# Kernel tuning notes

Hardware: AMD Instinct MI355X
Metric: run time of the kernel (lower is better)

Reference implementation:

```python
import jax, jax.numpy as jnp
import numpy as np

DIM = 512
NUM_HEADS = 16
WIN = (7, 7)
N = WIN[0] * WIN[1]          # 49 tokens per window
NW = 64                      # windows per image
B = 32                       # images
B_ = B * NW                  # total windows = 2048
SCALE = (DIM // NUM_HEADS) ** -0.5


def _relative_position_index(wh, ww):
    coords = np.stack(np.meshgrid(np.arange(wh), np.arange(ww), indexing='ij'))  # (2, wh, ww)
    coords = coords.reshape(2, -1)                                               # (2, N)
    rel = coords[:, :, None] - coords[:, None, :]                                # (2, N, N)
    rel = rel.transpose(1, 2, 0).astype(np.int32)                                # (N, N, 2)
    rel[:, :, 0] += wh - 1
    rel[:, :, 1] += ww - 1
    rel[:, :, 0] *= 2 * ww - 1
    return jnp.asarray(rel.sum(-1), dtype=jnp.int32)                             # (N, N)


def _shift_mask(nw, n):
    # Swin-style additive mask: 0 within groups, -100 across groups.
    rng = np.random.RandomState(0)
    groups = rng.randint(0, 4, size=(nw, n)).astype(np.int32)
    m = np.where(groups[:, :, None] == groups[:, None, :], 0.0, -100.0)
    return jnp.asarray(m, dtype=jnp.float32)                                     # (nW, N, N)


def setup_inputs() -> dict:
    key = jax.random.key(0)
    ks = jax.random.split(key, 5)
    x = jax.random.normal(ks[0], (B_, N, DIM), dtype=jnp.float32)
    qkv_w = jax.random.normal(ks[1], (3 * DIM, DIM), dtype=jnp.float32) * 0.02
    qkv_b = jnp.zeros((3 * DIM,), dtype=jnp.float32)
    proj_w = jax.random.normal(ks[2], (DIM, DIM), dtype=jnp.float32) * 0.02
    proj_b = jnp.zeros((DIM,), dtype=jnp.float32)
    rpb_table = jax.random.normal(ks[3], ((2 * WIN[0] - 1) * (2 * WIN[1] - 1), NUM_HEADS), dtype=jnp.float32) * 0.02
    mask = _shift_mask(NW, N)
    rel_idx = _relative_position_index(*WIN)
    return {"x": x, "mask": mask, "qkv_w": qkv_w, "qkv_b": qkv_b,
            "proj_w": proj_w, "proj_b": proj_b, "rpb_table": rpb_table,
            "rel_idx": rel_idx}


def reference(x, mask, qkv_w, qkv_b, proj_w, proj_b, rpb_table, rel_idx):
    b_, n, c = x.shape
    nh = rpb_table.shape[1]
    d = c // nh
    # qkv projection: (B_, N, 3, nH, d) -> q, k, v each (B_, nH, N, d)
    qkv = (jnp.einsum('bnc,oc->bno', x, qkv_w) + qkv_b).reshape(b_, n, 3, nh, d)
    qkv = jnp.transpose(qkv, (2, 0, 3, 1, 4))
    q, k, v = qkv[0], qkv[1], qkv[2]
    attn = jnp.einsum('bhnd,bhmd->bhnm', q * SCALE, k)                     # (B_, nH, N, N)
    # gathered relative position bias: (N*N, nH) -> (nH, N, N)
    bias = rpb_table[rel_idx.reshape(-1)].reshape(n, n, nh)
    attn = attn + jnp.transpose(bias, (2, 0, 1))[None]
    # shifted-window mask add
    nw = mask.shape[0]
    attn = attn.reshape(b_ // nw, nw, nh, n, n) + mask[None, :, None]
    attn = attn.reshape(b_, nh, n, n)
    attn = jax.nn.softmax(attn, axis=-1)
    out = jnp.einsum('bhnm,bhmd->bhnd', attn, v)                           # (B_, nH, N, d)
    out = jnp.transpose(out, (0, 2, 1, 3)).reshape(b_, n, c)
    return jnp.einsum('bnc,oc->bno', out, proj_w) + proj_b
```

## Files before the change

### kernel.cpp

```cpp
#include <hip/hip_runtime.h>
#include <hip/hip_bf16.h>
#include <stdint.h>
#include <stddef.h>

#define B_TOT   2048
#define NTOK    49
#define CDIM    512
#define NHEAD   16
#define HD      32
#define NWIN    64
#define MROWS   (B_TOT*NTOK)
#define O_QKV   1536
#define SCALE_F 0.17677669529663687f

typedef short bf16x8 __attribute__((ext_vector_type(8)));
typedef float f32x4  __attribute__((ext_vector_type(4)));

__device__ __forceinline__ unsigned short f2bf(float f){
  union { float f; unsigned u; } v; v.f = f;
  unsigned r = v.u + 0x7fffu + ((v.u >> 16) & 1u);
  return (unsigned short)(r >> 16);
}
__device__ __forceinline__ unsigned pkbf(float a, float b){
  return (unsigned)f2bf(a) | ((unsigned)f2bf(b) << 16);
}

#define GL16(g,l) __builtin_amdgcn_global_load_lds( \
      (const __attribute__((address_space(1))) unsigned int*)(g), \
      (__attribute__((address_space(3))) unsigned int*)(l), 16, 0, 0)

__global__ void k_prep(const float* __restrict__ x,
                       const float* __restrict__ qkv_w, const float* __restrict__ proj_w,
                       const float* __restrict__ rpb, const int* __restrict__ rel_idx,
                       const float* __restrict__ mask,
                       unsigned short* __restrict__ xb,
                       unsigned short* __restrict__ wqkv, unsigned short* __restrict__ wproj,
                       float* __restrict__ bmb){
  int i = blockIdx.x * blockDim.x + threadIdx.x;
  int st = gridDim.x * blockDim.x;
  const int n4 = MROWS * CDIM / 4;
  for (int j = i; j < n4; j += st){
    float4 v = ((const float4*)x)[j];
    uint2 o;
    o.x = pkbf(v.x, v.y);
    o.y = pkbf(v.z, v.w);
    ((uint2*)xb)[j] = o;
  }
  for (int j = i; j < O_QKV*CDIM; j += st) wqkv[j] = f2bf(qkv_w[j]);
  for (int j = i; j < CDIM*CDIM;  j += st) wproj[j] = f2bf(proj_w[j]);
  const int TOT = NWIN * NHEAD * NTOK * 64;
  for (int j = i; j < TOT; j += st){
    int wh  = j / (NTOK*64);
    int rem = j - wh * (NTOK*64);
    int qt  = rem >> 6, kt = rem & 63;
    int wi = wh >> 4, h = wh & 15;
    float v;
    if (kt < NTOK){
      int rc = qt * NTOK + kt;
      v = mask[wi * (NTOK*NTOK) + rc] + rpb[rel_idx[rc] * NHEAD + h];
    } else v = -1e30f;
    bmb[j] = v;
  }
}

#define LDA_(P,RG,MI,S) (*(const bf16x8*)(rA + (P)*32768 + (RG)*16384 + (MI)*2048 + ((S)?(cb0^64):cb0)))
#define LDB_(P,CG,NI,S) (*(const bf16x8*)(rB + (P)*32768 + (CG)*16384 + (NI)*2048 + ((S)?(cb0^64):cb0)))

#define RDA(P,RG)  { _Pragma("unroll") for (int mi=0;mi<4;++mi){ af[mi][0]=LDA_(P,RG,mi,0); af[mi][1]=LDA_(P,RG,mi,1);} }
#define RDB0(P,CG) { _Pragma("unroll") for (int ni=0;ni<2;++ni){ bfr0[ni][0]=LDB_(P,CG,ni,0); bfr0[ni][1]=LDB_(P,CG,ni,1);} }
#define RDB1(P,CG) { _Pragma("unroll") for (int ni=0;ni<2;++ni){ bfr1[ni][0]=LDB_(P,CG,ni,0); bfr1[ni][1]=LDB_(P,CG,ni,1);} }

#define STAGE_A(P,HG,KT) { \
    GL16(aS0 + (size_t)(HG)*64*Kb + (size_t)(KT)*128, ldA + (P)*32768 + (HG)*16384); \
    GL16(aS1 + (size_t)(HG)*64*Kb + (size_t)(KT)*128, ldA + (P)*32768 + (HG)*16384 + 8192); }
#define STAGE_B(P,HG,KT) { \
    GL16(bS0 + (size_t)(HG)*32*Kb + (size_t)(KT)*128, ldB + (P)*32768 + (HG)*16384); \
    GL16(bS1 + (size_t)(HG)*32*Kb + (size_t)(KT)*128, ldB + (P)*32768 + (HG)*16384 + 8192); }

#define PH2(PRE,RG,VM) { \
  PRE; \
  __builtin_amdgcn_s_barrier(); \
  asm volatile("s_waitcnt lgkmcnt(0)" ::: "memory"); \
  __builtin_amdgcn_sched_barrier(0); \
  __builtin_amdgcn_s_setprio(1); \
  _Pragma("unroll") for (int s=0;s<2;++s) \
    _Pragma("unroll") for (int mi=0;mi<4;++mi){ \
      _Pragma("unroll") for (int ni=0;ni<2;++ni) \
        acc[(RG)*4+mi][ni] = __builtin_amdgcn_mfma_f32_16x16x32_bf16(af[mi][s], bfr0[ni][s], acc[(RG)*4+mi][ni], 0,0,0); \
      _Pragma("unroll") for (int ni=0;ni<2;++ni) \
        acc[(RG)*4+mi][2+ni] = __builtin_amdgcn_mfma_f32_16x16x32_bf16(af[mi][s], bfr1[ni][s], acc[(RG)*4+mi][2+ni], 0,0,0); \
    } \
  __builtin_amdgcn_s_setprio(0); \
  if (VM) asm volatile("s_waitcnt vmcnt(4)" ::: "memory"); \
  __builtin_amdgcn_s_barrier(); \
  asm volatile("" ::: "memory"); \
}

template<int OUT_F32>
__global__ __launch_bounds__(512, 2) void k_gemm8(const unsigned short* __restrict__ Ag,
                                                  const unsigned short* __restrict__ Bg,
                                                  const float* __restrict__ bias,
                                                  void* __restrict__ Cout,
                                                  int Ndim, int Kdim){
  extern __shared__ char smem[];
  const int tid = threadIdx.x;
  const int wv = tid >> 6, lane = tid & 63, lg = lane >> 4, lr = lane & 15;
  const int wm = wv >> 2, wn = wv & 3;

  const int nbx = gridDim.x;
  const int nwg = nbx * gridDim.y;
  const int id  = blockIdx.y * nbx + blockIdx.x;
  const int nid = (id & 7) * (nwg >> 3) + (id >> 3);
  const int bx = nid % nbx, by = nid / nbx;
  const int bm0 = by * 256, bn0 = bx * 256;
  const size_t Kb = (size_t)Kdim * 2;
  const int NIT = Kdim >> 7;

  const int srow = tid >> 3;
  const int scb  = ((tid & 7) << 4) ^ ((srow & 7) << 4);
  const char* aS0 = (const char*)Ag + (size_t)(bm0 + srow) * Kb + scb;
  const char* aS1 = (const char*)Ag + (size_t)(bm0 + 128 + srow) * Kb + scb;
  const char* bS0 = (const char*)Bg + (size_t)(bn0 + (srow>>5)*64 + (srow&31)) * Kb + scb;
  const char* bS1 = (const char*)Bg + (size_t)(bn0 + 128 + (srow>>5)*64 + (srow&31)) * Kb + scb;
  char* ldA = smem + wv * 1024;
  char* ldB = smem + 65536 + wv * 1024;

  const int cb0 = (lg * 16) ^ ((lr & 7) << 4);
  const char* rA = smem + (wm*64 + lr) * 128;
  const char* rB = smem + 65536 + (wn*32 + lr) * 128;

  f32x4 acc[8][4];
  #pragma unroll
  for (int i = 0; i < 8; ++i)
    #pragma unroll
    for (int j = 0; j < 4; ++j)
      #pragma unroll
      for (int r = 0; r < 4; ++r) acc[i][j][r] = 0.f;

  bf16x8 af[4][2], bfr0[2][2], bfr1[2][2];

  STAGE_A(0,0,0); STAGE_A(0,1,0); STAGE_B(0,0,0); STAGE_B(0,1,0);
  STAGE_A(1,0,1); STAGE_B(1,1,1);
  asm volatile("s_waitcnt vmcnt(4)" ::: "memory");
  __builtin_amdgcn_s_barrier();
  asm volatile("" ::: "memory");

  for (int it = 0; it < NIT; ++it){
    const int T = 2*it;
    PH2( RDA(0,0); RDB0(0,0); RDB1(0,1); STAGE_A(1,1,(T+1)); STAGE_B(1,0,(T+1)), 0, 0)
    PH2( RDA(0,1); STAGE_A(0,0,(T+2)); STAGE_B(0,1,(T+2)),                        1, 1)
    PH2( RDA(1,0); RDB0(1,0); RDB1(1,1); STAGE_A(0,1,(T+2)); STAGE_B(0,0,(T+2)), 0, 0)
    PH2( RDA(1,1); STAGE_A(1,0,(T+3)); STAGE_B(1,1,(T+3)),                        1, 1)
  }

  #pragma unroll
  for (int RG = 0; RG < 2; ++RG)
    #pragma unroll
    for (int mi = 0; mi < 4; ++mi)
      #pragma unroll
      for (int CG = 0; CG < 2; ++CG)
        #pragma unroll
        for (int ni = 0; ni < 2; ++ni){
          f32x4 v = acc[RG*4+mi][CG*2+ni];
          const int col = bn0 + wn*64 + CG*32 + ni*16 + lr;
          const float bc = bias[col];
          #pragma unroll
          for (int r = 0; r < 4; ++r){
            const int row = bm0 + wm*128 + RG*64 + mi*16 + lg*4 + r;
            const float t = v[r] + bc;
            if (OUT_F32) ((float*)Cout)[(size_t)row * Ndim + col] = t;
            else ((unsigned short*)Cout)[(size_t)row * Ndim + col] = f2bf(t);
          }
        }
}

__global__ __launch_bounds__(256) void k_attn(const unsigned short* __restrict__ qkv,
                                              const float* __restrict__ bm,
                                              unsigned short* __restrict__ ao){
  __shared__ char lds[4][12288];
  const int wv = threadIdx.x >> 6, lane = threadIdx.x & 63;
  const int lg = lane >> 4, lr = lane & 15;
  const int gw = blockIdx.x * 4 + wv;
  const int w = gw >> 4, h = gw & 15, wi = w & (NWIN - 1);
  char* Vt = lds[wv];
  char* P  = lds[wv] + 4096;

  const unsigned short* base = qkv + (size_t)w * NTOK * O_QKV + h * HD;

  const int vkt = lane >> 2, vch = lane & 3;
  bf16x8 vld[4];
  #pragma unroll
  for (int t = 0; t < 4; ++t){
    int kt = 16*t + vkt; int kts = kt < NTOK ? kt : NTOK-1;
    vld[t] = *(const bf16x8*)(base + 1024 + (size_t)kts * O_QKV + vch * 8);
  }

  bf16x8 qf[4], kf[4];
  #pragma unroll
  for (int i = 0; i < 4; ++i){
    int t = 16*i + lr; int ts = t < NTOK ? t : NTOK-1;
    qf[i] = *(const bf16x8*)(base + (size_t)ts * O_QKV + lg*8);
    kf[i] = *(const bf16x8*)(base + 512 + (size_t)ts * O_QKV + lg*8);
  }

  const float* bmp = bm + (size_t)(wi * NHEAD + h) * (NTOK * 64);
  f32x4 bias[4][4];
  #pragma unroll
  for (int mi = 0; mi < 4; ++mi){
    int qt = 16*mi + lr; int qtc = qt < NTOK ? qt : NTOK-1;
    #pragma unroll
    for (int ni = 0; ni < 4; ++ni)
      bias[mi][ni] = *(const f32x4*)(bmp + qtc*64 + ni*16 + lg*4);
  }

  f32x4 z4 = {0.f, 0.f, 0.f, 0.f};
  f32x4 s2[4][4];
  #pragma unroll
  for (int ni = 0; ni < 4; ++ni)
    #pragma unroll
    for (int mi = 0; mi < 4; ++mi)
      s2[ni][mi] = __builtin_amdgcn_mfma_f32_16x16x32_bf16(kf[ni], qf[mi], z4, 0, 0, 0);

  #pragma unroll
  for (int t = 0; t < 4; ++t){
    int kt = 16*t + vkt;
    #pragma unroll
    for (int j = 0; j < 8; ++j){
      int d = vch*8 + j;
      int swz = ((d & 7) ^ (d >> 3)) & 7;
      int byte = d*128 + ((2*kt) ^ (swz << 4));
      *(unsigned short*)(Vt + byte) = (unsigned short)vld[t][j];
    }
  }

  #pragma unroll
  for (int mi = 0; mi < 4; ++mi){
    float v[4][4];
    float mx = -1e30f;
    #pragma unroll
    for (int ni = 0; ni < 4; ++ni)
      #pragma unroll
      for (int r = 0; r < 4; ++r){
        float t = s2[ni][mi][r] * SCALE_F + bias[mi][ni][r];
        v[ni][r] = t;
        mx = fmaxf(mx, t);
      }
    mx = fmaxf(mx, __shfl_xor(mx, 16));
    mx = fmaxf(mx, __shfl_xor(mx, 32));
    float sum = 0.f;
    #pragma unroll
    for (int ni = 0; ni < 4; ++ni)
      #pragma unroll
      for (int r = 0; r < 4; ++r){
        float p = __expf(v[ni][r] - mx);
        v[ni][r] = p;
        sum += p;
      }
    sum += __shfl_xor(sum, 16);
    sum += __shfl_xor(sum, 32);
    float rn = 1.0f / sum;
    const int qt = 16*mi + lr;
    #pragma unroll
    for (int ni = 0; ni < 4; ++ni){
      uint2 pw;
      pw.x = pkbf(v[ni][0]*rn, v[ni][1]*rn);
      pw.y = pkbf(v[ni][2]*rn, v[ni][3]*rn);
      int byte = qt*128 + ((32*ni + 8*lg) ^ ((lr & 7) << 4));
      *(uint2*)(P + byte) = pw;
    }
  }

  f32x4 o[4][2];
  #pragma unroll
  for (int mi = 0; mi < 4; ++mi)
    #pragma unroll
    for (int ni = 0; ni < 2; ++ni)
      #pragma unroll
      for (int r = 0; r < 4; ++r) o[mi][ni][r] = 0.f;

  #pragma unroll
  for (int s = 0; s < 2; ++s){
    bf16x8 pf[4], vf[2];
    #pragma unroll
    for (int mi = 0; mi < 4; ++mi)
      pf[mi] = *(const bf16x8*)(P + (16*mi + lr)*128 + ((64*s + 16*lg) ^ ((lr & 7) << 4)));
    #pragma unroll
    for (int ni = 0; ni < 2; ++ni){
      int d = 16*ni + lr;
      int swz = ((d & 7) ^ (d >> 3)) & 7;
      vf[ni] = *(const bf16x8*)(Vt + d*128 + ((64*s + 16*lg) ^ (swz << 4)));
    }
    #pragma unroll
    for (int mi = 0; mi < 4; ++mi)
      #pragma unroll
      for (int ni = 0; ni < 2; ++ni)
        o[mi][ni] = __builtin_amdgcn_mfma_f32_16x16x32_bf16(pf[mi], vf[ni], o[mi][ni], 0, 0, 0);
  }

  unsigned short* aop = ao + (size_t)w * NTOK * CDIM + h * HD;
  #pragma unroll
  for (int mi = 0; mi < 4; ++mi)
    #pragma unroll
    for (int ni = 0; ni < 2; ++ni)
      #pragma unroll
      for (int r = 0; r < 4; ++r){
        int row = 16*mi + 4*lg + r, col = 16*ni + lr;
        if (row < NTOK)
          aop[(size_t)row * CDIM + col] = f2bf(o[mi][ni][r]);
      }
}

extern "C" void kernel_launch(void* const* d_in, const int* in_sizes, int n_in,
                              void* d_out, int out_size, void* d_ws, size_t ws_size,
                              hipStream_t stream){
  const float* x      = (const float*)d_in[0];
  const float* mask   = (const float*)d_in[1];
  const float* qkv_w  = (const float*)d_in[2];
  const float* qkv_b  = (const float*)d_in[3];
  const float* proj_w = (const float*)d_in[4];
  const float* proj_b = (const float*)d_in[5];
  const float* rpb    = (const float*)d_in[6];
  const int*   rel_i  = (const int*)d_in[7];

  char* ws = (char*)d_ws;
  unsigned short* xb    = (unsigned short*)(ws);
  unsigned short* qkvb  = (unsigned short*)(ws + 102760448);
  unsigned short* wqkv  = (unsigned short*)(ws + 411041792);
  unsigned short* wproj = (unsigned short*)(ws + 412614656);
  float*          bmb   = (float*)(ws + 413138944);

  (void)hipFuncSetAttribute(reinterpret_cast<const void*>(&k_gemm8<0>),
                            hipFuncAttributeMaxDynamicSharedMemorySize, 131072);
  (void)hipFuncSetAttribute(reinterpret_cast<const void*>(&k_gemm8<1>),
                            hipFuncAttributeMaxDynamicSharedMemorySize, 131072);

  k_prep<<<2048, 256, 0, stream>>>(x, qkv_w, proj_w, rpb, rel_i, mask, xb, wqkv, wproj, bmb);
  k_gemm8<0><<<dim3(O_QKV/256, MROWS/256), 512, 131072, stream>>>(xb, wqkv, qkv_b, qkvb, O_QKV, CDIM);
  k_attn<<<(B_TOT * NHEAD) / 4, 256, 0, stream>>>(qkvb, bmb, xb);
  k_gemm8<1><<<dim3(CDIM/256, MROWS/256), 512, 131072, stream>>>(xb, wproj, proj_b, d_out, CDIM, CDIM);
}
```

Measured before the change: 494.8 us.

## Process two adjacent N-tiles per GEMM workgroup with prefetch across tiles

Each GEMM workgroup now computes two consecutive 256-wide output column tiles for the same row block, halving the grid. The last K iteration of the first tile prefetches the first K slices of the next tile's B operand, so the pipeline prologue is overlapped. The intent is to amortize launch/prologue cost and reuse A-row locality in cache, at the cost of fewer workgroups and longer per-block runtime. Correctness relies on the A tile restaging from K=0 and on N being a multiple of 512.

```diff
diff --git a/kernel.cpp b/kernel.cpp
--- a/kernel.cpp
+++ b/kernel.cpp
@@ -76,6 +76,9 @@
 #define STAGE_B(P,HG,KT) { \
     GL16(bS0 + (size_t)(HG)*32*Kb + (size_t)(KT)*128, ldB + (P)*32768 + (HG)*16384); \
     GL16(bS1 + (size_t)(HG)*32*Kb + (size_t)(KT)*128, ldB + (P)*32768 + (HG)*16384 + 8192); }
+#define STAGE_BN(P,HG,KT) { \
+    GL16(bS0 + offD + (size_t)(HG)*32*Kb + (size_t)(KT)*128, ldB + (P)*32768 + (HG)*16384); \
+    GL16(bS1 + offD + (size_t)(HG)*32*Kb + (size_t)(KT)*128, ldB + (P)*32768 + (HG)*16384 + 8192); }
 
 #define PH2(PRE,RG,VM) { \
   PRE; \
@@ -107,12 +110,13 @@
   const int wv = tid >> 6, lane = tid & 63, lg = lane >> 4, lr = lane & 15;
   const int wm = wv >> 2, wn = wv & 3;
 
-  const int nbx = gridDim.x;
-  const int nwg = nbx * gridDim.y;
-  const int id  = blockIdx.y * nbx + blockIdx.x;
-  const int nid = (id & 7) * (nwg >> 3) + (id >> 3);
-  const int bx = nid % nbx, by = nid / nbx;
-  const int bm0 = by * 256, bn0 = bx * 256;
+  const int npairs = gridDim.x;
+  const int b = blockIdx.x;
+  const int pid = (b & 7) * (npairs >> 3) + (b >> 3);
+  const int nbx = Ndim >> 8;
+  const int id0 = pid * 2;
+  const int bx0 = id0 % nbx, by = id0 / nbx;
+  const int bm0 = by * 256;
   const size_t Kb = (size_t)Kdim * 2;
   const int NIT = Kdim >> 7;
 
@@ -120,8 +124,9 @@
   const int scb  = ((tid & 7) << 4) ^ ((srow & 7) << 4);
   const char* aS0 = (const char*)Ag + (size_t)(bm0 + srow) * Kb + scb;
   const char* aS1 = (const char*)Ag + (size_t)(bm0 + 128 + srow) * Kb + scb;
-  const char* bS0 = (const char*)Bg + (size_t)(bn0 + (srow>>5)*64 + (srow&31)) * Kb + scb;
-  const char* bS1 = (const char*)Bg + (size_t)(bn0 + 128 + (srow>>5)*64 + (srow&31)) * Kb + scb;
+  const char* bS0 = (const char*)Bg + (size_t)((bx0 << 8) + (srow>>5)*64 + (srow&31)) * Kb + scb;
+  const char* bS1 = (const char*)Bg + (size_t)((bx0 << 8) + 128 + (srow>>5)*64 + (srow&31)) * Kb + scb;
+  size_t offD = (size_t)256 * Kb;
   char* ldA = smem + wv * 1024;
   char* ldB = smem + 65536 + wv * 1024;
 
@@ -130,13 +135,6 @@
   const char* rB = smem + 65536 + (wn*32 + lr) * 128;
 
   f32x4 acc[8][4];
-  #pragma unroll
-  for (int i = 0; i < 8; ++i)
-    #pragma unroll
-    for (int j = 0; j < 4; ++j)
-      #pragma unroll
-      for (int r = 0; r < 4; ++r) acc[i][j][r] = 0.f;
-
   bf16x8 af[4][2], bfr0[2][2], bfr1[2][2];
 
   STAGE_A(0,0,0); STAGE_A(0,1,0); STAGE_B(0,0,0); STAGE_B(0,1,0);
@@ -145,33 +143,54 @@
   __builtin_amdgcn_s_barrier();
   asm volatile("" ::: "memory");
 
-  for (int it = 0; it < NIT; ++it){
-    const int T = 2*it;
-    PH2( RDA(0,0); RDB0(0,0); RDB1(0,1); STAGE_A(1,1,(T+1)); STAGE_B(1,0,(T+1)), 0, 0)
-    PH2( RDA(0,1); STAGE_A(0,0,(T+2)); STAGE_B(0,1,(T+2)),                        1, 1)
-    PH2( RDA(1,0); RDB0(1,0); RDB1(1,1); STAGE_A(0,1,(T+2)); STAGE_B(0,0,(T+2)), 0, 0)
-    PH2( RDA(1,1); STAGE_A(1,0,(T+3)); STAGE_B(1,1,(T+3)),                        1, 1)
-  }
-
-  #pragma unroll
-  for (int RG = 0; RG < 2; ++RG)
-    #pragma unroll
-    for (int mi = 0; mi < 4; ++mi)
-      #pragma unroll
-      for (int CG = 0; CG < 2; ++CG)
+  for (int t = 0; t < 2; ++t){
+    #pragma unroll
+    for (int i = 0; i < 8; ++i)
+      #pragma unroll
+      for (int j = 0; j < 4; ++j)
         #pragma unroll
-        for (int ni = 0; ni < 2; ++ni){
-          f32x4 v = acc[RG*4+mi][CG*2+ni];
-          const int col = bn0 + wn*64 + CG*32 + ni*16 + lr;
-          const float bc = bias[col];
+        for (int r = 0; r < 4; ++r) acc[i][j][r] = 0.f;
+
+    for (int it = 0; it < NIT-1; ++it){
+      const int T = 2*it;
+      PH2( RDA(0,0); RDB0(0,0); RDB1(0,1); STAGE_A(1,1,(T+1)); STAGE_B(1,0,(T+1)), 0, 0)
+      PH2( RDA(0,1); STAGE_A(0,0,(T+2)); STAGE_B(0,1,(T+2)),                        1, 1)
+      PH2( RDA(1,0); RDB0(1,0); RDB1(1,1); STAGE_A(0,1,(T+2)); STAGE_B(0,0,(T+2)), 0, 0)
+      PH2( RDA(1,1); STAGE_A(1,0,(T+3)); STAGE_B(1,1,(T+3)),                        1, 1)
+    }
+    {
+      const int TL = 2*(NIT-1);
+      PH2( RDA(0,0); RDB0(0,0); RDB1(0,1); STAGE_A(1,1,(TL+1)); STAGE_B(1,0,(TL+1)), 0, 0)
+      PH2( RDA(0,1); STAGE_A(0,0,0); STAGE_BN(0,1,0),                                1, 1)
+      PH2( RDA(1,0); RDB0(1,0); RDB1(1,1); STAGE_A(0,1,0); STAGE_BN(0,0,0),          0, 0)
+      PH2( RDA(1,1); STAGE_A(1,0,1); STAGE_BN(1,1,1),                                1, 1)
+    }
+
+    const int bn0 = (bx0 + t) << 8;
+    #pragma unroll
+    for (int RG = 0; RG < 2; ++RG)
+      #pragma unroll
+      for (int mi = 0; mi < 4; ++mi)
+        #pragma unroll
+        for (int CG = 0; CG < 2; ++CG)
           #pragma unroll
-          for (int r = 0; r < 4; ++r){
-            const int row = bm0 + wm*128 + RG*64 + mi*16 + lg*4 + r;
-            const float t = v[r] + bc;
-            if (OUT_F32) ((float*)Cout)[(size_t)row * Ndim + col] = t;
-            else ((unsigned short*)Cout)[(size_t)row * Ndim + col] = f2bf(t);
+          for (int ni = 0; ni < 2; ++ni){
+            f32x4 v = acc[RG*4+mi][CG*2+ni];
+            const int col = bn0 + wn*64 + CG*32 + ni*16 + lr;
+            const float bc = bias[col];
+            #pragma unroll
+            for (int r = 0; r < 4; ++r){
+              const int row = bm0 + wm*128 + RG*64 + mi*16 + lg*4 + r;
+              const float tv = v[r] + bc;
+              if (OUT_F32) ((float*)Cout)[(size_t)row * Ndim + col] = tv;
+              else ((unsigned short*)Cout)[(size_t)row * Ndim + col] = f2bf(tv);
+            }
           }
-        }
+
+    bS0 += (size_t)256 * Kb;
+    bS1 += (size_t)256 * Kb;
+    offD = 0;
+  }
 }
 
 __global__ __launch_bounds__(256) void k_attn(const unsigned short* __restrict__ qkv,
@@ -335,7 +354,7 @@
                             hipFuncAttributeMaxDynamicSharedMemorySize, 131072);
 
   k_prep<<<2048, 256, 0, stream>>>(x, qkv_w, proj_w, rpb, rel_i, mask, xb, wqkv, wproj, bmb);
-  k_gemm8<0><<<dim3(O_QKV/256, MROWS/256), 512, 131072, stream>>>(xb, wqkv, qkv_b, qkvb, O_QKV, CDIM);
+  k_gemm8<0><<<1176, 512, 131072, stream>>>(xb, wqkv, qkv_b, qkvb, O_QKV, CDIM);
   k_attn<<<(B_TOT * NHEAD) / 4, 256, 0, stream>>>(qkvb, bmb, xb);
-  k_gemm8<1><<<dim3(CDIM/256, MROWS/256), 512, 131072, stream>>>(xb, wproj, proj_b, d_out, CDIM, CDIM);
-}
+  k_gemm8<1><<<392, 512, 131072, stream>>>(xb, wproj, proj_b, d_out, CDIM, CDIM);
+}
```

After: 708.1 us. +43.1%, slower.
